# Optimization experiments

Measured on AMD Instinct MI355X. Metric: run time of the kernel, lower is better.

## Reference

```python
import jax, jax.numpy as jnp
import numpy as np

EMBED = 1024

def setup_inputs() -> dict:
    key = jax.random.key(0)
    ks = jax.random.split(key, 10)
    B, S, E = 4, 2048, EMBED
    inv = 1.0 / np.sqrt(E)
    return {
        "query": jax.random.normal(ks[0], (B, S, E), jnp.float32),
        "key": jax.random.normal(ks[1], (B, S, E), jnp.float32),
        "value": jax.random.normal(ks[2], (B, S, E), jnp.float32),
        "attn_mask": jnp.zeros((B, S, S), jnp.float32),
        "Wq": jax.random.normal(ks[3], (E, E), jnp.float32) * inv,
        "bq": jnp.zeros((E,), jnp.float32),
        "Wk": jax.random.normal(ks[4], (E, E), jnp.float32) * inv,
        "bk": jnp.zeros((E,), jnp.float32),
        "Wv": jax.random.normal(ks[5], (E, E), jnp.float32) * inv,
        "bv": jnp.zeros((E,), jnp.float32),
    }

def reference(query, key, value, attn_mask, Wq, bq, Wk, bk, Wv, bv):
    E = query.shape[-1]
    q = query @ Wq.T + bq            # [B,S,E]
    k = key @ Wk.T + bk              # [B,S,E]
    v = value @ Wv.T + bv            # [B,S,E]
    scores = jnp.einsum('bse,bte->bst', q, k) / jnp.sqrt(jnp.float32(E))
    scores = scores + attn_mask      # [B,S,S]
    attn = jax.nn.softmax(scores, axis=-1)
    return jnp.einsum('bst,bte->bse', attn, v)
```

## Files before the change

kernel.cpp:

```cpp
#include <hip/hip_runtime.h>
#include <cstdint>
#include <cstddef>

typedef __bf16 bf16;
typedef __bf16 bf16x8 __attribute__((ext_vector_type(8)));
typedef float  f32x4  __attribute__((ext_vector_type(4)));

#define NB 4
#define SS 2048
#define EE 1024

#define BUFB  24576
#define LDS3  (3 * BUFB)
#define LDS6  (6 * BUFB)

static __device__ __forceinline__ void glds16(const bf16* g, void* l)
{
    __builtin_amdgcn_global_load_lds(
        (const __attribute__((address_space(1))) unsigned int*)g,
        (__attribute__((address_space(3))) unsigned int*)l,
        16, 0, 0);
}

static __device__ __forceinline__ void swz_block(int& bx, int& by, int& bz)
{
    const int nx = gridDim.x, ny = gridDim.y;
    const int nwg = nx * ny * gridDim.z;
    int lin = blockIdx.x + nx * (blockIdx.y + ny * blockIdx.z);
    const int per = nwg >> 3;
    lin = (lin & 7) * per + (lin >> 3);
    bz = lin / (nx * ny);
    const int r = lin - bz * nx * ny;
    by = r / nx;
    bx = r - by * nx;
}

template<int NBUF>
static __device__ __forceinline__ void kloop32(
    const bf16* __restrict__ A, const bf16* __restrict__ Bm,
    int lda, int ldb, int nt, char* lds, int m0, int n0, int tid,
    f32x4 acc[4][4])
{
    const int lane = tid & 63, w = tid >> 6;
    const int wm = w >> 2, wn = w & 3;
    const int lr = lane & 15, kq = lane >> 4;
    const int cb = (kq * 16) ^ ((lr & 3) << 4);

    const int srow   = tid >> 2;
    const int chunkL = (tid & 3) ^ (srow & 3);
    const bf16* Asrc = A  + (size_t)(m0 + srow) * lda + chunkL * 8;
    const bf16* Bsrc = Bm + (size_t)(n0 + srow) * ldb + chunkL * 8;
    const int wofs = w << 10;

#pragma unroll
    for (int p = 0; p < NBUF - 1; ++p) {
        char* d = lds + p * BUFB + wofs;
        const int kt = p * 32;
        glds16(Asrc + kt,                     d);
        glds16(Bsrc + kt,                     d + 8192);
        glds16(Bsrc + (size_t)128 * ldb + kt, d + 16384);
    }
    if constexpr (NBUF == 3) asm volatile("s_waitcnt vmcnt(3)" ::: "memory");
    else                     asm volatile("s_waitcnt vmcnt(12)" ::: "memory");
    __builtin_amdgcn_sched_barrier(0);
    __builtin_amdgcn_s_barrier();
    __builtin_amdgcn_sched_barrier(0);

    int rb = 0, sb = NBUF - 1;
    for (int t = 0; t < nt; ++t) {
        char* la = lds + rb * BUFB;
        char* lb = la + 8192;
        const int ts = (t + NBUF - 1 < nt) ? t + NBUF - 1 : nt - 1;
        const int kt = ts * 32;
        char* d = lds + sb * BUFB + wofs;

        bf16x8 af[4], bg[4];
#pragma unroll
        for (int m = 0; m < 4; ++m)
            af[m] = *(const bf16x8*)(la + (wm * 64 + m * 16 + lr) * 64 + cb);
#pragma unroll
        for (int n = 0; n < 4; ++n)
            bg[n] = *(const bf16x8*)(lb + (wn * 64 + n * 16 + lr) * 64 + cb);

        glds16(Asrc + kt,                     d);
        glds16(Bsrc + kt,                     d + 8192);
        glds16(Bsrc + (size_t)128 * ldb + kt, d + 16384);

        __builtin_amdgcn_s_setprio(1);
#pragma unroll
        for (int m = 0; m < 4; ++m)
#pragma unroll
            for (int n = 0; n < 4; ++n)
                acc[m][n] = __builtin_amdgcn_mfma_f32_16x16x32_bf16(af[m], bg[n], acc[m][n], 0, 0, 0);
        __builtin_amdgcn_s_setprio(0);

        if (t < nt - 1) {
            if constexpr (NBUF == 3) asm volatile("s_waitcnt vmcnt(3)" ::: "memory");
            else                     asm volatile("s_waitcnt vmcnt(12)" ::: "memory");
            __builtin_amdgcn_sched_barrier(0);
            __builtin_amdgcn_s_barrier();
            __builtin_amdgcn_sched_barrier(0);
        }
        rb = (rb + 1 == NBUF) ? 0 : rb + 1;
        sb = (sb + 1 == NBUF) ? 0 : sb + 1;
    }
    asm volatile("s_waitcnt vmcnt(0)" ::: "memory");
}

__global__ __launch_bounds__(256) void cvt3_kernel(
    const float* __restrict__ s0, const float* __restrict__ s1, const float* __restrict__ s2,
    bf16* __restrict__ d0, bf16* __restrict__ d1, bf16* __restrict__ d2, unsigned n)
{
    const float* s; bf16* d;
    if (blockIdx.y == 0)      { s = s0; d = d0; }
    else if (blockIdx.y == 1) { s = s1; d = d1; }
    else                      { s = s2; d = d2; }
    const size_t i = ((size_t)blockIdx.x * 256 + threadIdx.x) * 8;
    if (i >= n) return;
    const float4 f0 = *(const float4*)(s + i);
    const float4 f1 = *(const float4*)(s + i + 4);
    bf16x8 h;
    h[0] = (bf16)f0.x; h[1] = (bf16)f0.y; h[2] = (bf16)f0.z; h[3] = (bf16)f0.w;
    h[4] = (bf16)f1.x; h[5] = (bf16)f1.y; h[6] = (bf16)f1.z; h[7] = (bf16)f1.w;
    *(bf16x8*)(d + i) = h;
}

__global__ __launch_bounds__(512, 4) void proj8(
    const bf16* __restrict__ qc, const bf16* __restrict__ kc, const bf16* __restrict__ vc,
    const bf16* __restrict__ Wc,
    const float* __restrict__ bq, const float* __restrict__ bk, const float* __restrict__ bv,
    bf16* __restrict__ qb, bf16* __restrict__ kb, bf16* __restrict__ vb)
{
    extern __shared__ char lds[];
    int bx, by, bz; swz_block(bx, by, bz);
    const bf16* A; const float* bias; bf16* out;
    if (bz == 0)      { A = qc; bias = bq; out = qb; }
    else if (bz == 1) { A = kc; bias = bk; out = kb; }
    else              { A = vc; bias = bv; out = vb; }
    const bf16* Bm = Wc + (size_t)bz * EE * EE;

    const int m0 = by * 128, n0 = bx * 256;
    const int tid = threadIdx.x;

    f32x4 acc[4][4];
#pragma unroll
    for (int m = 0; m < 4; ++m)
#pragma unroll
        for (int n = 0; n < 4; ++n) { acc[m][n][0] = 0.f; acc[m][n][1] = 0.f; acc[m][n][2] = 0.f; acc[m][n][3] = 0.f; }

    kloop32<3>(A, Bm, EE, EE, EE / 32, lds, m0, n0, tid, acc);

    const int lane = tid & 63, w = tid >> 6, wm = w >> 2, wn = w & 3;
    const int lr = lane & 15, kq = lane >> 4;
#pragma unroll
    for (int n = 0; n < 4; ++n) {
        const int gcol = n0 + wn * 64 + n * 16 + lr;
        const float bb = bias[gcol];
#pragma unroll
        for (int m = 0; m < 4; ++m)
#pragma unroll
            for (int j = 0; j < 4; ++j) {
                const int grow = m0 + wm * 64 + m * 16 + kq * 4 + j;
                out[(size_t)grow * EE + gcol] = (bf16)(acc[m][n][j] + bb);
            }
    }
}

__global__ __launch_bounds__(256) void transpose_kernel(const bf16* __restrict__ vb,
                                                        bf16* __restrict__ vt)
{
    __shared__ bf16 t[64][72];
    const int b  = blockIdx.z;
    const int s0 = blockIdx.x * 64, e0 = blockIdx.y * 64;
    const int tid = threadIdx.x;

    const bf16* src = vb + ((size_t)b * SS + s0) * EE + e0;
#pragma unroll
    for (int i = 0; i < 2; ++i) {
        const int c  = tid * 2 + i;
        const int r  = c >> 3;
        const int cc = (c & 7) * 8;
        *(uint4*)&t[r][cc] = *(const uint4*)&src[(size_t)r * EE + cc];
    }
    __syncthreads();

    bf16* dst = vt + ((size_t)b * EE + e0) * SS + s0;
    const int er  = tid >> 2;
    const int sc0 = (tid & 3) * 16;
    bf16 tmp[16];
#pragma unroll
    for (int k2 = 0; k2 < 16; ++k2) tmp[k2] = t[sc0 + k2][er];
    *(uint4*)&dst[(size_t)er * SS + sc0]     = *(uint4*)&tmp[0];
    *(uint4*)&dst[(size_t)er * SS + sc0 + 8] = *(uint4*)&tmp[8];
}

__global__ __launch_bounds__(512, 4) void scores8(const bf16* __restrict__ qb,
                                                  const bf16* __restrict__ kb,
                                                  const float* __restrict__ mask,
                                                  bf16* __restrict__ sc)
{
    extern __shared__ char lds[];
    int bx, by, bz; swz_block(bx, by, bz);
    const bf16* A  = qb + (size_t)bz * SS * EE;
    const bf16* Bm = kb + (size_t)bz * SS * EE;

    const int m0 = by * 128, n0 = bx * 256;
    const int tid = threadIdx.x;

    f32x4 acc[4][4];
#pragma unroll
    for (int m = 0; m < 4; ++m)
#pragma unroll
        for (int n = 0; n < 4; ++n) { acc[m][n][0] = 0.f; acc[m][n][1] = 0.f; acc[m][n][2] = 0.f; acc[m][n][3] = 0.f; }

    kloop32<3>(A, Bm, EE, EE, EE / 32, lds, m0, n0, tid, acc);

    const int lane = tid & 63, w = tid >> 6, wm = w >> 2, wn = w & 3;
    const int lr = lane & 15, kq = lane >> 4;
    const float* mrow = mask + (size_t)bz * SS * SS;
    bf16* out = sc + (size_t)bz * SS * SS;
    const float scale = 0.03125f;
#pragma unroll
    for (int m = 0; m < 4; ++m)
#pragma unroll
        for (int n = 0; n < 4; ++n)
#pragma unroll
            for (int j = 0; j < 4; ++j) {
                const int grow = m0 + wm * 64 + m * 16 + kq * 4 + j;
                const int gcol = n0 + wn * 64 + n * 16 + lr;
                const float v = acc[m][n][j] * scale + mrow[(size_t)grow * SS + gcol];
                out[(size_t)grow * SS + gcol] = (bf16)v;
            }
}

__global__ __launch_bounds__(256) void softmax_kernel(bf16* __restrict__ sc)
{
    __shared__ float red[4];
    const size_t row = blockIdx.x;
    uint4* rp = (uint4*)(sc + row * (size_t)SS);
    const int tid = threadIdx.x, lane = tid & 63, wid = tid >> 6;

    const uint4 d = rp[tid];
    const unsigned int u[4] = { d.x, d.y, d.z, d.w };
    float f[8];
#pragma unroll
    for (int i = 0; i < 4; ++i) {
        union { unsigned int i_; float f_; } lo, hi;
        lo.i_ = u[i] << 16;
        hi.i_ = u[i] & 0xffff0000u;
        f[2 * i]     = lo.f_;
        f[2 * i + 1] = hi.f_;
    }

    float m = f[0];
#pragma unroll
    for (int i = 1; i < 8; ++i) m = fmaxf(m, f[i]);
#pragma unroll
    for (int o = 32; o > 0; o >>= 1) m = fmaxf(m, __shfl_xor(m, o));
    if (lane == 0) red[wid] = m;
    __syncthreads();
    m = fmaxf(fmaxf(red[0], red[1]), fmaxf(red[2], red[3]));
    __syncthreads();

    float e[8], s = 0.f;
#pragma unroll
    for (int i = 0; i < 8; ++i) { e[i] = __expf(f[i] - m); s += e[i]; }
#pragma unroll
    for (int o = 32; o > 0; o >>= 1) s += __shfl_xor(s, o);
    if (lane == 0) red[wid] = s;
    __syncthreads();
    s = red[0] + red[1] + red[2] + red[3];
    const float inv = 1.0f / s;

    unsigned int ou[4];
#pragma unroll
    for (int i = 0; i < 4; ++i) {
        union { bf16 h; unsigned short b; } a0, a1;
        a0.h = (bf16)(e[2 * i] * inv);
        a1.h = (bf16)(e[2 * i + 1] * inv);
        ou[i] = ((unsigned int)a1.b << 16) | (unsigned int)a0.b;
    }
    rp[tid] = make_uint4(ou[0], ou[1], ou[2], ou[3]);
}

__global__ __launch_bounds__(512, 2) void pv8(const bf16* __restrict__ sc,
                                              const bf16* __restrict__ vt,
                                              float* __restrict__ outp)
{
    extern __shared__ char lds[];
    int bx, by, bz; swz_block(bx, by, bz);
    const bf16* A  = sc + (size_t)bz * SS * SS;
    const bf16* Bm = vt + (size_t)bz * EE * SS;

    const int m0 = by * 128, n0 = bx * 256;
    const int tid = threadIdx.x;

    f32x4 acc[4][4];
#pragma unroll
    for (int m = 0; m < 4; ++m)
#pragma unroll
        for (int n = 0; n < 4; ++n) { acc[m][n][0] = 0.f; acc[m][n][1] = 0.f; acc[m][n][2] = 0.f; acc[m][n][3] = 0.f; }

    kloop32<6>(A, Bm, SS, SS, SS / 32, lds, m0, n0, tid, acc);

    const int lane = tid & 63, w = tid >> 6, wm = w >> 2, wn = w & 3;
    const int lr = lane & 15, kq = lane >> 4;
#pragma unroll
    for (int m = 0; m < 4; ++m)
#pragma unroll
        for (int n = 0; n < 4; ++n)
#pragma unroll
            for (int j = 0; j < 4; ++j) {
                const int grow = m0 + wm * 64 + m * 16 + kq * 4 + j;
                const int gcol = n0 + wn * 64 + n * 16 + lr;
                outp[((size_t)bz * SS + grow) * EE + gcol] = acc[m][n][j];
            }
}

extern "C" void kernel_launch(void* const* d_in, const int* in_sizes, int n_in,
                              void* d_out, int out_size, void* d_ws, size_t ws_size,
                              hipStream_t stream)
{
    const float* query = (const float*)d_in[0];
    const float* key_  = (const float*)d_in[1];
    const float* value = (const float*)d_in[2];
    const float* mask  = (const float*)d_in[3];
    const float* Wq = (const float*)d_in[4];
    const float* bq = (const float*)d_in[5];
    const float* Wk = (const float*)d_in[6];
    const float* bk = (const float*)d_in[7];
    const float* Wv = (const float*)d_in[8];
    const float* bv = (const float*)d_in[9];
    float* outp = (float*)d_out;

    char* ws = (char*)d_ws;
    const size_t QKV = (size_t)NB * SS * EE * 2;
    const size_t SCB = (size_t)NB * SS * SS * 2;
    const size_t WCB = (size_t)3 * EE * EE * 2;
    if (ws_size < 4 * QKV + SCB + WCB) return;

    bf16* qb = (bf16*)(ws);
    bf16* kb = (bf16*)(ws + QKV);
    bf16* vb = (bf16*)(ws + 2 * QKV);
    bf16* vt = (bf16*)(ws + 3 * QKV);
    bf16* sc = (bf16*)(ws + 4 * QKV);
    bf16* Wc = (bf16*)(ws + 4 * QKV + SCB);
    bf16* qc = vt;
    bf16* kc = sc;
    bf16* vc = (bf16*)(ws + 5 * QKV);

    (void)hipFuncSetAttribute((const void*)proj8,   hipFuncAttributeMaxDynamicSharedMemorySize, LDS3);
    (void)hipFuncSetAttribute((const void*)scores8, hipFuncAttributeMaxDynamicSharedMemorySize, LDS3);
    (void)hipFuncSetAttribute((const void*)pv8,     hipFuncAttributeMaxDynamicSharedMemorySize, LDS6);

    dim3 blk(256), blk5(512);
    const unsigned NQKV = (unsigned)NB * SS * EE;
    const unsigned NW   = (unsigned)EE * EE;
    cvt3_kernel<<<dim3(NQKV / (256 * 8), 3), blk, 0, stream>>>(
        query, key_, value, qc, kc, vc, NQKV);
    cvt3_kernel<<<dim3(NW / (256 * 8), 3), blk, 0, stream>>>(
        Wq, Wk, Wv, Wc, Wc + (size_t)EE * EE, Wc + 2 * (size_t)EE * EE, NW);

    proj8<<<dim3(EE / 256, (NB * SS) / 128, 3), blk5, LDS3, stream>>>(
        qc, kc, vc, Wc, bq, bk, bv, qb, kb, vb);
    transpose_kernel<<<dim3(SS / 64, EE / 64, NB), blk, 0, stream>>>(vb, vt);
    scores8<<<dim3(SS / 256, SS / 128, NB), blk5, LDS3, stream>>>(qb, kb, mask, sc);
    softmax_kernel<<<dim3(NB * SS), blk, 0, stream>>>(sc);
    pv8<<<dim3(EE / 256, SS / 128, NB), blk5, LDS6, stream>>>(sc, vt, outp);
}
```

Before: 203.6 us.

## Generalize GEMM k-loop to templated tiles with split A-fragment MFMA phases

Replaces the fixed 128x256 GEMM mainloop with a templated kernel parameterised by M/N repetition. It uses a 4-stage LDS ring and a new XOR-swizzled 128-byte-line LDS layout, and splits each k-step into two MFMA halves with global-to-LDS loads interleaved between them. The QK^T scores GEMM grows to 256x256 tiles and the projection switches to 256x128 tiles to increase operand reuse per block. Occupancy bounds drop to 2 blocks per CU to fit the larger accumulators and LDS buffers, which reduces latency hiding.

New measurement: 210.4 us. +3.3%, slower.

```diff
diff --git a/kernel.cpp b/kernel.cpp
--- a/kernel.cpp
+++ b/kernel.cpp
@@ -9,10 +9,6 @@
 #define NB 4
 #define SS 2048
 #define EE 1024
-
-#define BUFB  24576
-#define LDS3  (3 * BUFB)
-#define LDS6  (6 * BUFB)
 
 static __device__ __forceinline__ void glds16(const bf16* g, void* l)
 {
@@ -35,33 +31,51 @@
     bx = r - by * nx;
 }
 
-template<int NBUF>
-static __device__ __forceinline__ void kloop32(
+template<int M_REP, int N_REP>
+static __device__ __forceinline__ void kloopX(
     const bf16* __restrict__ A, const bf16* __restrict__ Bm,
     int lda, int ldb, int nt, char* lds, int m0, int n0, int tid,
-    f32x4 acc[4][4])
-{
+    f32x4 acc[M_REP][N_REP])
+{
+    constexpr int BM = 32 * M_REP, BN = 64 * N_REP;
+    constexpr int AREG = BM * 64;
+    constexpr int BUFB = (BM + BN) * 64;
+    constexpr int LA = BM / 128, LB = BN / 128, L = LA + LB;
+    constexpr int NBUF = 4;
+    constexpr int MH = M_REP / 2;
+
     const int lane = tid & 63, w = tid >> 6;
     const int wm = w >> 2, wn = w & 3;
     const int lr = lane & 15, kq = lane >> 4;
-    const int cb = (kq * 16) ^ ((lr & 3) << 4);
-
-    const int srow   = tid >> 2;
-    const int chunkL = (tid & 3) ^ (srow & 3);
-    const bf16* Asrc = A  + (size_t)(m0 + srow) * lda + chunkL * 8;
-    const bf16* Bsrc = Bm + (size_t)(n0 + srow) * ldb + chunkL * 8;
+    const int lby  = (lr >> 1) * 128 + (((kq + 4 * (lr & 1)) ^ (lr >> 1)) << 4);
+    const int aoff = wm * (M_REP * 1024) + lby;
+    const int boff = AREG + wn * (N_REP * 1024) + lby;
     const int wofs = w << 10;
+
+    const bf16* pA[LA];
+    const bf16* pB[LB];
+#pragma unroll
+    for (int i = 0; i < LA; ++i) {
+        const int idx = i * 512 + tid, line = idx >> 3, u = (idx & 7) ^ (line & 7);
+        pA[i] = A + (size_t)(m0 + 2 * line + (u >> 2)) * lda + (u & 3) * 8;
+    }
+#pragma unroll
+    for (int i = 0; i < LB; ++i) {
+        const int idx = i * 512 + tid, line = idx >> 3, u = (idx & 7) ^ (line & 7);
+        pB[i] = Bm + (size_t)(n0 + 2 * line + (u >> 2)) * ldb + (u & 3) * 8;
+    }
 
 #pragma unroll
     for (int p = 0; p < NBUF - 1; ++p) {
         char* d = lds + p * BUFB + wofs;
         const int kt = p * 32;
-        glds16(Asrc + kt,                     d);
-        glds16(Bsrc + kt,                     d + 8192);
-        glds16(Bsrc + (size_t)128 * ldb + kt, d + 16384);
-    }
-    if constexpr (NBUF == 3) asm volatile("s_waitcnt vmcnt(3)" ::: "memory");
-    else                     asm volatile("s_waitcnt vmcnt(12)" ::: "memory");
+#pragma unroll
+        for (int i = 0; i < LA; ++i) glds16(pA[i] + kt, d + i * 8192);
+#pragma unroll
+        for (int i = 0; i < LB; ++i) glds16(pB[i] + kt, d + AREG + i * 8192);
+    }
+    if constexpr (L == 3) asm volatile("s_waitcnt vmcnt(6)" ::: "memory");
+    else                  asm volatile("s_waitcnt vmcnt(8)" ::: "memory");
     __builtin_amdgcn_sched_barrier(0);
     __builtin_amdgcn_s_barrier();
     __builtin_amdgcn_sched_barrier(0);
@@ -69,34 +83,46 @@
     int rb = 0, sb = NBUF - 1;
     for (int t = 0; t < nt; ++t) {
         char* la = lds + rb * BUFB;
-        char* lb = la + 8192;
-        const int ts = (t + NBUF - 1 < nt) ? t + NBUF - 1 : nt - 1;
+        const int ts = (t + NBUF - 1 < nt) ? (t + NBUF - 1) : (nt - 1);
         const int kt = ts * 32;
         char* d = lds + sb * BUFB + wofs;
 
-        bf16x8 af[4], bg[4];
-#pragma unroll
-        for (int m = 0; m < 4; ++m)
-            af[m] = *(const bf16x8*)(la + (wm * 64 + m * 16 + lr) * 64 + cb);
-#pragma unroll
-        for (int n = 0; n < 4; ++n)
-            bg[n] = *(const bf16x8*)(lb + (wn * 64 + n * 16 + lr) * 64 + cb);
-
-        glds16(Asrc + kt,                     d);
-        glds16(Bsrc + kt,                     d + 8192);
-        glds16(Bsrc + (size_t)128 * ldb + kt, d + 16384);
+        bf16x8 bg[N_REP], af[MH];
+#pragma unroll
+        for (int n = 0; n < N_REP; ++n)
+            bg[n] = *(const bf16x8*)(la + boff + n * 1024);
+#pragma unroll
+        for (int m = 0; m < MH; ++m)
+            af[m] = *(const bf16x8*)(la + aoff + m * 1024);
+#pragma unroll
+        for (int i = 0; i < LA; ++i) glds16(pA[i] + kt, d + i * 8192);
 
         __builtin_amdgcn_s_setprio(1);
 #pragma unroll
-        for (int m = 0; m < 4; ++m)
-#pragma unroll
-            for (int n = 0; n < 4; ++n)
+        for (int m = 0; m < MH; ++m)
+#pragma unroll
+            for (int n = 0; n < N_REP; ++n)
                 acc[m][n] = __builtin_amdgcn_mfma_f32_16x16x32_bf16(af[m], bg[n], acc[m][n], 0, 0, 0);
         __builtin_amdgcn_s_setprio(0);
 
+        bf16x8 ag[MH];
+#pragma unroll
+        for (int m = 0; m < MH; ++m)
+            ag[m] = *(const bf16x8*)(la + aoff + (MH + m) * 1024);
+#pragma unroll
+        for (int i = 0; i < LB; ++i) glds16(pB[i] + kt, d + AREG + i * 8192);
+
+        __builtin_amdgcn_s_setprio(1);
+#pragma unroll
+        for (int m = 0; m < MH; ++m)
+#pragma unroll
+            for (int n = 0; n < N_REP; ++n)
+                acc[MH + m][n] = __builtin_amdgcn_mfma_f32_16x16x32_bf16(ag[m], bg[n], acc[MH + m][n], 0, 0, 0);
+        __builtin_amdgcn_s_setprio(0);
+
         if (t < nt - 1) {
-            if constexpr (NBUF == 3) asm volatile("s_waitcnt vmcnt(3)" ::: "memory");
-            else                     asm volatile("s_waitcnt vmcnt(12)" ::: "memory");
+            if constexpr (L == 3) asm volatile("s_waitcnt vmcnt(6)" ::: "memory");
+            else                  asm volatile("s_waitcnt vmcnt(8)" ::: "memory");
             __builtin_amdgcn_sched_barrier(0);
             __builtin_amdgcn_s_barrier();
             __builtin_amdgcn_sched_barrier(0);
@@ -125,7 +151,7 @@
     *(bf16x8*)(d + i) = h;
 }
 
-__global__ __launch_bounds__(512, 4) void proj8(
+__global__ __launch_bounds__(512, 2) void proj8(
     const bf16* __restrict__ qc, const bf16* __restrict__ kc, const bf16* __restrict__ vc,
     const bf16* __restrict__ Wc,
     const float* __restrict__ bq, const float* __restrict__ bk, const float* __restrict__ bv,
@@ -139,28 +165,28 @@
     else              { A = vc; bias = bv; out = vb; }
     const bf16* Bm = Wc + (size_t)bz * EE * EE;
 
-    const int m0 = by * 128, n0 = bx * 256;
+    const int m0 = by * 256, n0 = bx * 128;
     const int tid = threadIdx.x;
 
-    f32x4 acc[4][4];
-#pragma unroll
-    for (int m = 0; m < 4; ++m)
-#pragma unroll
-        for (int n = 0; n < 4; ++n) { acc[m][n][0] = 0.f; acc[m][n][1] = 0.f; acc[m][n][2] = 0.f; acc[m][n][3] = 0.f; }
-
-    kloop32<3>(A, Bm, EE, EE, EE / 32, lds, m0, n0, tid, acc);
+    f32x4 acc[8][2];
+#pragma unroll
+    for (int m = 0; m < 8; ++m)
+#pragma unroll
+        for (int n = 0; n < 2; ++n) { acc[m][n][0] = 0.f; acc[m][n][1] = 0.f; acc[m][n][2] = 0.f; acc[m][n][3] = 0.f; }
+
+    kloopX<8, 2>(A, Bm, EE, EE, EE / 32, lds, m0, n0, tid, acc);
 
     const int lane = tid & 63, w = tid >> 6, wm = w >> 2, wn = w & 3;
     const int lr = lane & 15, kq = lane >> 4;
 #pragma unroll
-    for (int n = 0; n < 4; ++n) {
-        const int gcol = n0 + wn * 64 + n * 16 + lr;
+    for (int n = 0; n < 2; ++n) {
+        const int gcol = n0 + wn * 32 + n * 16 + lr;
         const float bb = bias[gcol];
 #pragma unroll
-        for (int m = 0; m < 4; ++m)
+        for (int m = 0; m < 8; ++m)
 #pragma unroll
             for (int j = 0; j < 4; ++j) {
-                const int grow = m0 + wm * 64 + m * 16 + kq * 4 + j;
+                const int grow = m0 + wm * 128 + m * 16 + kq * 4 + j;
                 out[(size_t)grow * EE + gcol] = (bf16)(acc[m][n][j] + bb);
             }
     }
@@ -194,7 +220,7 @@
     *(uint4*)&dst[(size_t)er * SS + sc0 + 8] = *(uint4*)&tmp[8];
 }
 
-__global__ __launch_bounds__(512, 4) void scores8(const bf16* __restrict__ qb,
+__global__ __launch_bounds__(512, 2) void scores8(const bf16* __restrict__ qb,
                                                   const bf16* __restrict__ kb,
                                                   const float* __restrict__ mask,
                                                   bf16* __restrict__ sc)
@@ -204,16 +230,16 @@
     const bf16* A  = qb + (size_t)bz * SS * EE;
     const bf16* Bm = kb + (size_t)bz * SS * EE;
 
-    const int m0 = by * 128, n0 = bx * 256;
+    const int m0 = by * 256, n0 = bx * 256;
     const int tid = threadIdx.x;
 
-    f32x4 acc[4][4];
-#pragma unroll
-    for (int m = 0; m < 4; ++m)
+    f32x4 acc[8][4];
+#pragma unroll
+    for (int m = 0; m < 8; ++m)
 #pragma unroll
         for (int n = 0; n < 4; ++n) { acc[m][n][0] = 0.f; acc[m][n][1] = 0.f; acc[m][n][2] = 0.f; acc[m][n][3] = 0.f; }
 
-    kloop32<3>(A, Bm, EE, EE, EE / 32, lds, m0, n0, tid, acc);
+    kloopX<8, 4>(A, Bm, EE, EE, EE / 32, lds, m0, n0, tid, acc);
 
     const int lane = tid & 63, w = tid >> 6, wm = w >> 2, wn = w & 3;
     const int lr = lane & 15, kq = lane >> 4;
@@ -221,12 +247,12 @@
     bf16* out = sc + (size_t)bz * SS * SS;
     const float scale = 0.03125f;
 #pragma unroll
-    for (int m = 0; m < 4; ++m)
+    for (int m = 0; m < 8; ++m)
 #pragma unroll
         for (int n = 0; n < 4; ++n)
 #pragma unroll
             for (int j = 0; j < 4; ++j) {
-                const int grow = m0 + wm * 64 + m * 16 + kq * 4 + j;
+                const int grow = m0 + wm * 128 + m * 16 + kq * 4 + j;
                 const int gcol = n0 + wn * 64 + n * 16 + lr;
                 const float v = acc[m][n][j] * scale + mrow[(size_t)grow * SS + gcol];
                 out[(size_t)grow * SS + gcol] = (bf16)v;
@@ -301,7 +327,7 @@
 #pragma unroll
         for (int n = 0; n < 4; ++n) { acc[m][n][0] = 0.f; acc[m][n][1] = 0.f; acc[m][n][2] = 0.f; acc[m][n][3] = 0.f; }
 
-    kloop32<6>(A, Bm, SS, SS, SS / 32, lds, m0, n0, tid, acc);
+    kloopX<4, 4>(A, Bm, SS, SS, SS / 32, lds, m0, n0, tid, acc);
 
     const int lane = tid & 63, w = tid >> 6, wm = w >> 2, wn = w & 3;
     const int lr = lane & 15, kq = lane >> 4;
@@ -349,9 +375,12 @@
     bf16* kc = sc;
     bf16* vc = (bf16*)(ws + 5 * QKV);
 
-    (void)hipFuncSetAttribute((const void*)proj8,   hipFuncAttributeMaxDynamicSharedMemorySize, LDS3);
-    (void)hipFuncSetAttribute((const void*)scores8, hipFuncAttributeMaxDynamicSharedMemorySize, LDS3);
-    (void)hipFuncSetAttribute((const void*)pv8,     hipFuncAttributeMaxDynamicSharedMemorySize, LDS6);
+    const int LDS_PROJ   = 4 * (256 + 128) * 64;
+    const int LDS_SCORES = 4 * (256 + 256) * 64;
+    const int LDS_PV     = 4 * (128 + 256) * 64;
+    (void)hipFuncSetAttribute((const void*)proj8,   hipFuncAttributeMaxDynamicSharedMemorySize, LDS_PROJ);
+    (void)hipFuncSetAttribute((const void*)scores8, hipFuncAttributeMaxDynamicSharedMemorySize, LDS_SCORES);
+    (void)hipFuncSetAttribute((const void*)pv8,     hipFuncAttributeMaxDynamicSharedMemorySize, LDS_PV);
 
     dim3 blk(256), blk5(512);
     const unsigned NQKV = (unsigned)NB * SS * EE;
@@ -361,10 +390,10 @@
     cvt3_kernel<<<dim3(NW / (256 * 8), 3), blk, 0, stream>>>(
         Wq, Wk, Wv, Wc, Wc + (size_t)EE * EE, Wc + 2 * (size_t)EE * EE, NW);
 
-    proj8<<<dim3(EE / 256, (NB * SS) / 128, 3), blk5, LDS3, stream>>>(
+    proj8<<<dim3(EE / 128, (NB * SS) / 256, 3), blk5, LDS_PROJ, stream>>>(
         qc, kc, vc, Wc, bq, bk, bv, qb, kb, vb);
     transpose_kernel<<<dim3(SS / 64, EE / 64, NB), blk, 0, stream>>>(vb, vt);
-    scores8<<<dim3(SS / 256, SS / 128, NB), blk5, LDS3, stream>>>(qb, kb, mask, sc);
+    scores8<<<dim3(SS / 256, SS / 256, NB), blk5, LDS_SCORES, stream>>>(qb, kb, mask, sc);
     softmax_kernel<<<dim3(NB * SS), blk, 0, stream>>>(sc);
-    pv8<<<dim3(EE / 256, SS / 128, NB), blk5, LDS6, stream>>>(sc, vt, outp);
-}
+    pv8<<<dim3(EE / 256, SS / 128, NB), blk5, LDS_PV, stream>>>(sc, vt, outp);
+}
```

## Replace GEMM k-loop with 256x256 tiles, K=64 steps, and quarter-phase pipelining

Applied to the files above, without the earlier changes.

Rewrites the shared GEMM main loop to use K=64 slices, split A/B half-tiles with separate staggered global-to-LDS loads, an 8-way XOR swizzle, and four MFMA quarter-phases separated by barriers, in the style of a ping-pong schedule. Projection and score kernels move to 256x256 output tiles (MR=8) at occupancy 2 to raise arithmetic intensity, while PV keeps 128x256 tiles with the new loop. The cost targeted is global/LDS traffic per flop and load latency exposed between MFMA bursts. In exchange it adds more barriers per iteration, more accumulator registers, and lower occupancy.

Measured after the change: 201.1 us. Within noise of the previous version (-1.2%).

```diff
diff --git a/kernel.cpp b/kernel.cpp
--- a/kernel.cpp
+++ b/kernel.cpp
@@ -9,10 +9,6 @@
 #define NB 4
 #define SS 2048
 #define EE 1024
-
-#define BUFB  24576
-#define LDS3  (3 * BUFB)
-#define LDS6  (6 * BUFB)
 
 static __device__ __forceinline__ void glds16(const bf16* g, void* l)
 {
@@ -35,76 +31,133 @@
     bx = r - by * nx;
 }
 
-template<int NBUF>
-static __device__ __forceinline__ void kloop32(
+template<int MR>
+static __device__ __forceinline__ void kloop4(
     const bf16* __restrict__ A, const bf16* __restrict__ Bm,
     int lda, int ldb, int nt, char* lds, int m0, int n0, int tid,
-    f32x4 acc[4][4])
-{
+    f32x4 acc[MR][4])
+{
+    constexpr int RA    = MR * 16;
+    constexpr int SZA   = RA * 128;
+    constexpr int LA_H  = SZA / 8192;
+    constexpr int ABASE = 4 * SZA;
+    constexpr int SZB   = 16384;
+    constexpr int MH    = MR / 2;
+
     const int lane = tid & 63, w = tid >> 6;
     const int wm = w >> 2, wn = w & 3;
     const int lr = lane & 15, kq = lane >> 4;
-    const int cb = (kq * 16) ^ ((lr & 3) << 4);
-
-    const int srow   = tid >> 2;
-    const int chunkL = (tid & 3) ^ (srow & 3);
-    const bf16* Asrc = A  + (size_t)(m0 + srow) * lda + chunkL * 8;
-    const bf16* Bsrc = Bm + (size_t)(n0 + srow) * ldb + chunkL * 8;
+
+    const int k0x  = ((kq ^ (lr & 7)) << 4);
+    const int k1x  = (((4 + kq) ^ (lr & 7)) << 4);
+    const int arow = wm * (RA / 2) * 128 + lr * 128;
+    const int brow = wn * 32 * 128 + lr * 128;
     const int wofs = w << 10;
 
-#pragma unroll
-    for (int p = 0; p < NBUF - 1; ++p) {
-        char* d = lds + p * BUFB + wofs;
-        const int kt = p * 32;
-        glds16(Asrc + kt,                     d);
-        glds16(Bsrc + kt,                     d + 8192);
-        glds16(Bsrc + (size_t)128 * ldb + kt, d + 16384);
-    }
-    if constexpr (NBUF == 3) asm volatile("s_waitcnt vmcnt(3)" ::: "memory");
-    else                     asm volatile("s_waitcnt vmcnt(12)" ::: "memory");
+    const int srow = tid >> 3;
+    const int scol = ((tid & 7) ^ (srow & 7)) * 8;
+    const bf16* pA = A  + (size_t)(m0 + srow) * lda + scol;
+    const bf16* pB = Bm + (size_t)(n0 + srow) * ldb + scol;
+
+    auto stageA = [&](int t, int h) {
+        char* d = lds + ((2 * t + h) & 3) * SZA + wofs;
+        const bf16* s = pA + (size_t)(h * RA) * lda + t * 64;
+#pragma unroll
+        for (int i = 0; i < LA_H; ++i)
+            glds16(s + (size_t)(i * 64) * lda, d + i * 8192);
+    };
+    auto stageB = [&](int t, int h) {
+        char* d = lds + ABASE + ((2 * t + h) & 3) * SZB + wofs;
+        const bf16* s = pB + (size_t)(h * 128) * ldb + t * 64;
+        glds16(s, d);
+        glds16(s + (size_t)64 * ldb, d + 8192);
+    };
+    auto sync_pre = [] {
+        __builtin_amdgcn_sched_barrier(0);
+        __builtin_amdgcn_s_barrier();
+        asm volatile("s_waitcnt lgkmcnt(0)" ::: "memory");
+        __builtin_amdgcn_sched_barrier(0);
+        __builtin_amdgcn_s_setprio(1);
+    };
+    auto sync_post = [] {
+        __builtin_amdgcn_s_setprio(0);
+        __builtin_amdgcn_sched_barrier(0);
+        __builtin_amdgcn_s_barrier();
+    };
+
+    stageA(0, 0); stageA(0, 1); stageB(0, 0); stageB(0, 1);
+    stageA(1, 0); stageB(1, 0); stageA(1, 1);
+    if constexpr (MR == 8) asm volatile("s_waitcnt vmcnt(6)" ::: "memory");
+    else                   asm volatile("s_waitcnt vmcnt(4)" ::: "memory");
     __builtin_amdgcn_sched_barrier(0);
     __builtin_amdgcn_s_barrier();
-    __builtin_amdgcn_sched_barrier(0);
-
-    int rb = 0, sb = NBUF - 1;
+
+    bf16x8 af[MR], b0[4], b1[4];
+
+#define MFMA_Q(AOFF, BOFF, BARR) \
+    _Pragma("unroll") \
+    for (int mf = 0; mf < MH; ++mf) \
+        _Pragma("unroll") \
+        for (int nf = 0; nf < 2; ++nf) { \
+            acc[(AOFF) + mf][(BOFF) + nf] = __builtin_amdgcn_mfma_f32_16x16x32_bf16(af[2*mf],   BARR[2*nf],   acc[(AOFF) + mf][(BOFF) + nf], 0, 0, 0); \
+            acc[(AOFF) + mf][(BOFF) + nf] = __builtin_amdgcn_mfma_f32_16x16x32_bf16(af[2*mf+1], BARR[2*nf+1], acc[(AOFF) + mf][(BOFF) + nf], 0, 0, 0); \
+        }
+
     for (int t = 0; t < nt; ++t) {
-        char* la = lds + rb * BUFB;
-        char* lb = la + 8192;
-        const int ts = (t + NBUF - 1 < nt) ? t + NBUF - 1 : nt - 1;
-        const int kt = ts * 32;
-        char* d = lds + sb * BUFB + wofs;
-
-        bf16x8 af[4], bg[4];
-#pragma unroll
-        for (int m = 0; m < 4; ++m)
-            af[m] = *(const bf16x8*)(la + (wm * 64 + m * 16 + lr) * 64 + cb);
-#pragma unroll
-        for (int n = 0; n < 4; ++n)
-            bg[n] = *(const bf16x8*)(lb + (wn * 64 + n * 16 + lr) * 64 + cb);
-
-        glds16(Asrc + kt,                     d);
-        glds16(Bsrc + kt,                     d + 8192);
-        glds16(Bsrc + (size_t)128 * ldb + kt, d + 16384);
-
-        __builtin_amdgcn_s_setprio(1);
-#pragma unroll
-        for (int m = 0; m < 4; ++m)
-#pragma unroll
-            for (int n = 0; n < 4; ++n)
-                acc[m][n] = __builtin_amdgcn_mfma_f32_16x16x32_bf16(af[m], bg[n], acc[m][n], 0, 0, 0);
+        const int t1 = (t + 1 < nt) ? t + 1 : nt - 1;
+        const int t2 = (t + 2 < nt) ? t + 2 : nt - 1;
+        char* as0 = lds + ((2 * t)     & 3) * SZA;
+        char* as1 = lds + ((2 * t + 1) & 3) * SZA;
+        char* bs0 = lds + ABASE + ((2 * t)     & 3) * SZB;
+        char* bs1 = lds + ABASE + ((2 * t + 1) & 3) * SZB;
+
+#pragma unroll
+        for (int mf = 0; mf < MH; ++mf) {
+            af[2*mf]   = *(const bf16x8*)(as0 + arow + mf * 2048 + k0x);
+            af[2*mf+1] = *(const bf16x8*)(as0 + arow + mf * 2048 + k1x);
+        }
+#pragma unroll
+        for (int nf = 0; nf < 2; ++nf) {
+            b0[2*nf]   = *(const bf16x8*)(bs0 + brow + nf * 2048 + k0x);
+            b0[2*nf+1] = *(const bf16x8*)(bs0 + brow + nf * 2048 + k1x);
+        }
+        stageB(t1, 1);
+        sync_pre();
+        MFMA_Q(0, 0, b0)
+        sync_post();
+
+#pragma unroll
+        for (int nf = 0; nf < 2; ++nf) {
+            b1[2*nf]   = *(const bf16x8*)(bs1 + brow + nf * 2048 + k0x);
+            b1[2*nf+1] = *(const bf16x8*)(bs1 + brow + nf * 2048 + k1x);
+        }
+        stageA(t2, 0);
+        sync_pre();
+        MFMA_Q(0, 2, b1)
+        sync_post();
+
+#pragma unroll
+        for (int mf = 0; mf < MH; ++mf) {
+            af[2*mf]   = *(const bf16x8*)(as1 + arow + mf * 2048 + k0x);
+            af[2*mf+1] = *(const bf16x8*)(as1 + arow + mf * 2048 + k1x);
+        }
+        stageB(t2, 0);
+        sync_pre();
+        MFMA_Q(MH, 0, b0)
+        sync_post();
+
+        stageA(t2, 1);
+        sync_pre();
+        MFMA_Q(MH, 2, b1)
         __builtin_amdgcn_s_setprio(0);
-
-        if (t < nt - 1) {
-            if constexpr (NBUF == 3) asm volatile("s_waitcnt vmcnt(3)" ::: "memory");
-            else                     asm volatile("s_waitcnt vmcnt(12)" ::: "memory");
-            __builtin_amdgcn_sched_barrier(0);
-            __builtin_amdgcn_s_barrier();
-            __builtin_amdgcn_sched_barrier(0);
-        }
-        rb = (rb + 1 == NBUF) ? 0 : rb + 1;
-        sb = (sb + 1 == NBUF) ? 0 : sb + 1;
+        __builtin_amdgcn_sched_barrier(0);
+        if constexpr (MR == 8) asm volatile("s_waitcnt vmcnt(6)" ::: "memory");
+        else                   asm volatile("s_waitcnt vmcnt(4)" ::: "memory");
+        __builtin_amdgcn_sched_barrier(0);
+        __builtin_amdgcn_s_barrier();
     }
     asm volatile("s_waitcnt vmcnt(0)" ::: "memory");
+#undef MFMA_Q
 }
 
 __global__ __launch_bounds__(256) void cvt3_kernel(
@@ -125,7 +178,7 @@
     *(bf16x8*)(d + i) = h;
 }
 
-__global__ __launch_bounds__(512, 4) void proj8(
+__global__ __launch_bounds__(512, 2) void proj8(
     const bf16* __restrict__ qc, const bf16* __restrict__ kc, const bf16* __restrict__ vc,
     const bf16* __restrict__ Wc,
     const float* __restrict__ bq, const float* __restrict__ bk, const float* __restrict__ bv,
@@ -139,30 +192,33 @@
     else              { A = vc; bias = bv; out = vb; }
     const bf16* Bm = Wc + (size_t)bz * EE * EE;
 
-    const int m0 = by * 128, n0 = bx * 256;
+    const int m0 = by * 256, n0 = bx * 256;
     const int tid = threadIdx.x;
 
-    f32x4 acc[4][4];
-#pragma unroll
-    for (int m = 0; m < 4; ++m)
+    f32x4 acc[8][4];
+#pragma unroll
+    for (int m = 0; m < 8; ++m)
 #pragma unroll
         for (int n = 0; n < 4; ++n) { acc[m][n][0] = 0.f; acc[m][n][1] = 0.f; acc[m][n][2] = 0.f; acc[m][n][3] = 0.f; }
 
-    kloop32<3>(A, Bm, EE, EE, EE / 32, lds, m0, n0, tid, acc);
+    kloop4<8>(A, Bm, EE, EE, EE / 64, lds, m0, n0, tid, acc);
 
     const int lane = tid & 63, w = tid >> 6, wm = w >> 2, wn = w & 3;
     const int lr = lane & 15, kq = lane >> 4;
 #pragma unroll
-    for (int n = 0; n < 4; ++n) {
-        const int gcol = n0 + wn * 64 + n * 16 + lr;
+    for (int bi = 0; bi < 4; ++bi) {
+        const int nh = bi >> 1, nf = bi & 1;
+        const int gcol = n0 + nh * 128 + wn * 32 + nf * 16 + lr;
         const float bb = bias[gcol];
 #pragma unroll
-        for (int m = 0; m < 4; ++m)
+        for (int ai = 0; ai < 8; ++ai) {
+            const int mh = ai >> 2, mf = ai & 3;
 #pragma unroll
             for (int j = 0; j < 4; ++j) {
-                const int grow = m0 + wm * 64 + m * 16 + kq * 4 + j;
-                out[(size_t)grow * EE + gcol] = (bf16)(acc[m][n][j] + bb);
+                const int grow = m0 + mh * 128 + wm * 64 + mf * 16 + kq * 4 + j;
+                out[(size_t)grow * EE + gcol] = (bf16)(acc[ai][bi][j] + bb);
             }
+        }
     }
 }
 
@@ -194,7 +250,7 @@
     *(uint4*)&dst[(size_t)er * SS + sc0 + 8] = *(uint4*)&tmp[8];
 }
 
-__global__ __launch_bounds__(512, 4) void scores8(const bf16* __restrict__ qb,
+__global__ __launch_bounds__(512, 2) void scores8(const bf16* __restrict__ qb,
                                                   const bf16* __restrict__ kb,
                                                   const float* __restrict__ mask,
                                                   bf16* __restrict__ sc)
@@ -204,16 +260,16 @@
     const bf16* A  = qb + (size_t)bz * SS * EE;
     const bf16* Bm = kb + (size_t)bz * SS * EE;
 
-    const int m0 = by * 128, n0 = bx * 256;
+    const int m0 = by * 256, n0 = bx * 256;
     const int tid = threadIdx.x;
 
-    f32x4 acc[4][4];
-#pragma unroll
-    for (int m = 0; m < 4; ++m)
+    f32x4 acc[8][4];
+#pragma unroll
+    for (int m = 0; m < 8; ++m)
 #pragma unroll
         for (int n = 0; n < 4; ++n) { acc[m][n][0] = 0.f; acc[m][n][1] = 0.f; acc[m][n][2] = 0.f; acc[m][n][3] = 0.f; }
 
-    kloop32<3>(A, Bm, EE, EE, EE / 32, lds, m0, n0, tid, acc);
+    kloop4<8>(A, Bm, EE, EE, EE / 64, lds, m0, n0, tid, acc);
 
     const int lane = tid & 63, w = tid >> 6, wm = w >> 2, wn = w & 3;
     const int lr = lane & 15, kq = lane >> 4;
@@ -221,16 +277,20 @@
     bf16* out = sc + (size_t)bz * SS * SS;
     const float scale = 0.03125f;
 #pragma unroll
-    for (int m = 0; m < 4; ++m)
-#pragma unroll
-        for (int n = 0; n < 4; ++n)
+    for (int ai = 0; ai < 8; ++ai) {
+        const int mh = ai >> 2, mf = ai & 3;
+#pragma unroll
+        for (int bi = 0; bi < 4; ++bi) {
+            const int nh = bi >> 1, nf = bi & 1;
+            const int gcol = n0 + nh * 128 + wn * 32 + nf * 16 + lr;
 #pragma unroll
             for (int j = 0; j < 4; ++j) {
-                const int grow = m0 + wm * 64 + m * 16 + kq * 4 + j;
-                const int gcol = n0 + wn * 64 + n * 16 + lr;
-                const float v = acc[m][n][j] * scale + mrow[(size_t)grow * SS + gcol];
+                const int grow = m0 + mh * 128 + wm * 64 + mf * 16 + kq * 4 + j;
+                const float v = acc[ai][bi][j] * scale + mrow[(size_t)grow * SS + gcol];
                 out[(size_t)grow * SS + gcol] = (bf16)v;
             }
+        }
+    }
 }
 
 __global__ __launch_bounds__(256) void softmax_kernel(bf16* __restrict__ sc)
@@ -301,20 +361,24 @@
 #pragma unroll
         for (int n = 0; n < 4; ++n) { acc[m][n][0] = 0.f; acc[m][n][1] = 0.f; acc[m][n][2] = 0.f; acc[m][n][3] = 0.f; }
 
-    kloop32<6>(A, Bm, SS, SS, SS / 32, lds, m0, n0, tid, acc);
+    kloop4<4>(A, Bm, SS, SS, SS / 64, lds, m0, n0, tid, acc);
 
     const int lane = tid & 63, w = tid >> 6, wm = w >> 2, wn = w & 3;
     const int lr = lane & 15, kq = lane >> 4;
 #pragma unroll
-    for (int m = 0; m < 4; ++m)
-#pragma unroll
-        for (int n = 0; n < 4; ++n)
+    for (int ai = 0; ai < 4; ++ai) {
+        const int mh = ai >> 1, mf = ai & 1;
+#pragma unroll
+        for (int bi = 0; bi < 4; ++bi) {
+            const int nh = bi >> 1, nf = bi & 1;
+            const int gcol = n0 + nh * 128 + wn * 32 + nf * 16 + lr;
 #pragma unroll
             for (int j = 0; j < 4; ++j) {
-                const int grow = m0 + wm * 64 + m * 16 + kq * 4 + j;
-                const int gcol = n0 + wn * 64 + n * 16 + lr;
-                outp[((size_t)bz * SS + grow) * EE + gcol] = acc[m][n][j];
+                const int grow = m0 + mh * 64 + wm * 32 + mf * 16 + kq * 4 + j;
+                outp[((size_t)bz * SS + grow) * EE + gcol] = acc[ai][bi][j];
             }
+        }
+    }
 }
 
 extern "C" void kernel_launch(void* const* d_in, const int* in_sizes, int n_in,
@@ -349,9 +413,11 @@
     bf16* kc = sc;
     bf16* vc = (bf16*)(ws + 5 * QKV);
 
-    (void)hipFuncSetAttribute((const void*)proj8,   hipFuncAttributeMaxDynamicSharedMemorySize, LDS3);
-    (void)hipFuncSetAttribute((const void*)scores8, hipFuncAttributeMaxDynamicSharedMemorySize, LDS3);
-    (void)hipFuncSetAttribute((const void*)pv8,     hipFuncAttributeMaxDynamicSharedMemorySize, LDS6);
+    const int LDS8 = 4 * (128 * 128) + 4 * 16384;
+    const int LDS4 = 4 * (64 * 128)  + 4 * 16384;
+    (void)hipFuncSetAttribute((const void*)proj8,   hipFuncAttributeMaxDynamicSharedMemorySize, LDS8);
+    (void)hipFuncSetAttribute((const void*)scores8, hipFuncAttributeMaxDynamicSharedMemorySize, LDS8);
+    (void)hipFuncSetAttribute((const void*)pv8,     hipFuncAttributeMaxDynamicSharedMemorySize, LDS4);
 
     dim3 blk(256), blk5(512);
     const unsigned NQKV = (unsigned)NB * SS * EE;
@@ -361,10 +427,10 @@
     cvt3_kernel<<<dim3(NW / (256 * 8), 3), blk, 0, stream>>>(
         Wq, Wk, Wv, Wc, Wc + (size_t)EE * EE, Wc + 2 * (size_t)EE * EE, NW);
 
-    proj8<<<dim3(EE / 256, (NB * SS) / 128, 3), blk5, LDS3, stream>>>(
+    proj8<<<dim3(EE / 256, (NB * SS) / 256, 3), blk5, LDS8, stream>>>(
         qc, kc, vc, Wc, bq, bk, bv, qb, kb, vb);
     transpose_kernel<<<dim3(SS / 64, EE / 64, NB), blk, 0, stream>>>(vb, vt);
-    scores8<<<dim3(SS / 256, SS / 128, NB), blk5, LDS3, stream>>>(qb, kb, mask, sc);
+    scores8<<<dim3(SS / 256, SS / 256, NB), blk5, LDS8, stream>>>(qb, kb, mask, sc);
     softmax_kernel<<<dim3(NB * SS), blk, 0, stream>>>(sc);
-    pv8<<<dim3(EE / 256, SS / 128, NB), blk5, LDS6, stream>>>(sc, vt, outp);
-}
+    pv8<<<dim3(EE / 256, SS / 128, NB), blk5, LDS4, stream>>>(sc, vt, outp);
+}
```
